# Optimization experiments

Measured on AMD Instinct MI355X. Metric: run time of the kernel, lower is better.

The kernel has to match this reference:

```python
import jax, jax.numpy as jnp
import numpy as np

B, N, DIM = 4, 2048, 512
H, DH = 8, 64  # n_heads, dim_head; inner = H*DH = 512
SCALE = DH ** -0.5


def setup_inputs() -> dict:
    key = jax.random.key(0)
    k1, k2, k3 = jax.random.split(key, 3)
    inner = H * DH
    X = jax.random.normal(k1, (B, N, DIM), dtype=jnp.float32)
    W_qkv = jax.random.normal(k2, (DIM, 3 * inner), dtype=jnp.float32) * (DIM ** -0.5)
    W_out = jax.random.normal(k3, (inner, DIM), dtype=jnp.float32) * (inner ** -0.5)
    b_out = jnp.zeros((DIM,), dtype=jnp.float32)
    return {"X": X, "W_qkv": W_qkv, "W_out": W_out, "b_out": b_out}


def reference(X, W_qkv, W_out, b_out):
    # X: (b, n, dim)
    qkv = X @ W_qkv                      # (b, n, 3*h*d)
    q, k, v = jnp.split(qkv, 3, axis=-1)
    def to_heads(t):
        b, n, _ = t.shape
        return t.reshape(b, n, H, DH).transpose(0, 2, 1, 3)  # (b, h, n, d)
    q, k, v = to_heads(q), to_heads(k), to_heads(v)
    # NOTE: original computes scores[n, m] = k_n . q_m and softmaxes over m (query axis)
    scores = jnp.einsum('bhnd,bhmd->bhnm', k, q) * SCALE     # (b, h, n_k, m_q)
    att = jax.nn.softmax(scores, axis=-1)
    # out token axis is the KEY index n: out[n, d] = sum_e att[n, e] * v[e, d]
    out = jnp.einsum('bhne,bhed->bhnd', att, v)              # (b, h, n, d)
    out = out.transpose(0, 2, 1, 3).reshape(X.shape[0], X.shape[1], H * DH)  # (b, n, h*d)
    return out @ W_out + b_out
```

## Files before the change

### kernel.cpp

```cpp
#include <hip/hip_runtime.h>
#include <hip/hip_bf16.h>

typedef __bf16 bf16_t;
typedef bf16_t bf16x8 __attribute__((ext_vector_type(8)));
typedef bf16_t bf16x4v __attribute__((ext_vector_type(4)));
typedef float f32x4 __attribute__((ext_vector_type(4)));

#define B_SZ 4
#define N_TOK 2048
#define DIM 512
#define H_N 8
#define DH 64
#define INNER 512
#define M_ROWS 8192
#define NQKV 1536
#define K_FOLD 0.18033688011112042f

#define GLD_LDS16(gp, lp)                                          \
  __builtin_amdgcn_global_load_lds(                                \
      (const __attribute__((address_space(1))) void*)(gp),         \
      (__attribute__((address_space(3))) void*)(lp), 16, 0, 0)

__device__ __forceinline__ float fexp2(float x) {
#if __has_builtin(__builtin_amdgcn_exp2f)
  return __builtin_amdgcn_exp2f(x);
#else
  float r;
  asm volatile("v_exp_f32 %0, %1\n\ts_nop 1" : "=v"(r) : "v"(x));
  return r;
#endif
}


__global__ void f32_to_bf16_kernel(const float* __restrict__ src,
                                   bf16_t* __restrict__ dst, int n4) {
  int i = blockIdx.x * blockDim.x + threadIdx.x;
  int stride = gridDim.x * blockDim.x;
  for (; i < n4; i += stride) {
    float4 f = reinterpret_cast<const float4*>(src)[i];
    bf16x4v o;
    o.x = (bf16_t)f.x; o.y = (bf16_t)f.y; o.z = (bf16_t)f.z; o.w = (bf16_t)f.w;
    reinterpret_cast<bf16x4v*>(dst)[i] = o;
  }
}

__global__ void transpose_f32_to_bf16_kernel(const float* __restrict__ src,
                                             bf16_t* __restrict__ dst, int R, int C) {
  int t = blockIdx.x * blockDim.x + threadIdx.x;
  if (t >= R * C) return;
  int r = t / C, c = t - r * C;
  dst[(size_t)c * R + r] = (bf16_t)src[t];
}

template <int MODE>
__global__ __launch_bounds__(256) void gemm_bf16_kernel(
    const bf16_t* __restrict__ A, const bf16_t* __restrict__ Bt,
    int M, int Nn, int K,
    bf16_t* __restrict__ qb, bf16_t* __restrict__ kb, bf16_t* __restrict__ vb,
    float* __restrict__ outF, const float* __restrict__ bias) {
  __shared__ bf16_t As[128 * 64];
  __shared__ bf16_t Bs[128 * 64];

  const int tid = threadIdx.x;
  const int lane = tid & 63;
  const int wave = tid >> 6;
  const int g = lane >> 4, c = lane & 15;
  const int wm = (wave >> 1) * 64, wn = (wave & 1) * 64;
  const int m0 = blockIdx.x * 128, n0 = blockIdx.y * 128;

  f32x4 acc[4][4] = {};

  for (int k0 = 0; k0 < K; k0 += 64) {
    __syncthreads();
    #pragma unroll
    for (int i = 0; i < 4; ++i) {
      int blk = i * 256 + tid;
      int row = blk >> 3;
      int cb = (blk & 7) ^ (row & 7);
      int base = (i * 256 + wave * 64) * 8;
      GLD_LDS16(A + (size_t)(m0 + row) * K + k0 + cb * 8, &As[base]);
      GLD_LDS16(Bt + (size_t)(n0 + row) * K + k0 + cb * 8, &Bs[base]);
    }
    __syncthreads();
    __builtin_amdgcn_s_setprio(1);
    #pragma unroll
    for (int ks = 0; ks < 2; ++ks) {
      bf16x8 af[4], bfr[4];
      #pragma unroll
      for (int i = 0; i < 4; ++i) {
        af[i] = *reinterpret_cast<const bf16x8*>(
            &As[(wm + i * 16 + c) * 64 + (((ks * 4 + g) ^ (c & 7)) * 8)]);
        bfr[i] = *reinterpret_cast<const bf16x8*>(
            &Bs[(wn + i * 16 + c) * 64 + (((ks * 4 + g) ^ (c & 7)) * 8)]);
      }
      #pragma unroll
      for (int mi = 0; mi < 4; ++mi)
        #pragma unroll
        for (int ni = 0; ni < 4; ++ni)
          acc[mi][ni] = __builtin_amdgcn_mfma_f32_16x16x32_bf16(
              af[mi], bfr[ni], acc[mi][ni], 0, 0, 0);
    }
    __builtin_amdgcn_s_setprio(0);
  }

  #pragma unroll
  for (int mi = 0; mi < 4; ++mi) {
    #pragma unroll
    for (int ni = 0; ni < 4; ++ni) {
      int colg = n0 + wn + ni * 16 + c;
      #pragma unroll
      for (int r = 0; r < 4; ++r) {
        int rowg = m0 + wm + mi * 16 + g * 4 + r;
        float val = acc[mi][ni][r];
        if (MODE == 0) {
          int s = colg >> 9, cc2 = colg & 511;
          int hh = cc2 >> 6, dd = cc2 & 63;
          int bb = rowg >> 11, nn = rowg & 2047;
          if (s == 1) val *= K_FOLD;
          bf16_t* dst = (s == 0) ? qb : (s == 1) ? kb : vb;
          dst[(((size_t)(bb * H_N + hh)) * N_TOK + nn) * DH + dd] = (bf16_t)val;
        } else {
          outF[(size_t)rowg * Nn + colg] = val + bias[colg];
        }
      }
    }
  }
}

__global__ __launch_bounds__(256) void vtrans_kernel(const bf16_t* __restrict__ V,
                                                     bf16_t* __restrict__ Vt) {
  const int nb = blockIdx.x, bh = blockIdx.y;
  const bf16_t* src = V + (size_t)bh * N_TOK * DH;
  bf16_t* dst = Vt + (size_t)bh * DH * N_TOK;
  __shared__ bf16_t t[64][64];
  const int tid = threadIdx.x;
  #pragma unroll
  for (int i = 0; i < 2; ++i) {
    int idx = tid + 256 * i;
    int r = idx >> 3, j = idx & 7;
    int cx = (j ^ (r & 7) ^ (r >> 3)) * 8;
    *reinterpret_cast<uint4*>(&t[r][cx]) =
        *reinterpret_cast<const uint4*>(&src[(size_t)(nb * 64 + r) * DH + j * 8]);
  }
  __syncthreads();
  #pragma unroll
  for (int i = 0; i < 2; ++i) {
    int idx = tid + 256 * i;
    int d = idx >> 3, jn = idx & 7;
    bf16_t tmp[8];
    #pragma unroll
    for (int q = 0; q < 8; ++q)
      tmp[q] = t[jn * 8 + q][(((d >> 3) ^ q ^ jn) * 8) | (d & 7)];
    *reinterpret_cast<uint4*>(&dst[(size_t)d * N_TOK + nb * 64 + jn * 8]) =
        *reinterpret_cast<const uint4*>(tmp);
  }
}

__global__ __launch_bounds__(512, 4) void attn_kernel(
    const bf16_t* __restrict__ Qproj, const bf16_t* __restrict__ Kproj,
    const bf16_t* __restrict__ Vt, bf16_t* __restrict__ att_out) {
  const int glin = blockIdx.x;
  const int xcd = glin & 7;
  const int j = glin >> 3;
  const int hb = xcd * 4 + (j >> 4);
  const int rb = j & 15;
  const int h = hb & 7, b = hb >> 3;

  const size_t hbo = (size_t)(b * H_N + h);
  const bf16_t* Aq = Kproj + hbo * N_TOK * DH;
  const bf16_t* Ak = Qproj + hbo * N_TOK * DH;
  const bf16_t* Av = Vt + hbo * (size_t)DH * N_TOK;

  const int tid = threadIdx.x, lane = tid & 63, wave = tid >> 6;
  const int g = lane >> 4, c = lane & 15;
  const int r0 = rb * 128, wr0 = wave * 16;

  __shared__ bf16_t sK[2][64 * 64];
  __shared__ bf16_t sV[2][64 * 64];
  __shared__ bf16_t sP[8][16 * 72];

  bf16x8 qreg[2];
  #pragma unroll
  for (int ks = 0; ks < 2; ++ks)
    qreg[ks] = *reinterpret_cast<const bf16x8*>(
        &Aq[(size_t)(r0 + wr0 + c) * DH + ks * 32 + g * 8]);

  f32x4 accO[4] = {};
  float Lp[4] = {0.f, 0.f, 0.f, 0.f};

  auto stage = [&](int buf, int j0) {
    int row = tid >> 3;
    int cb = (tid & 7) ^ (row & 7);
    GLD_LDS16(Ak + (size_t)(j0 + row) * DH + cb * 8, &sK[buf][wave * 512]);
    GLD_LDS16(Av + (size_t)row * N_TOK + j0 + cb * 8, &sV[buf][wave * 512]);
  };

  stage(0, 0);
  __syncthreads();
  int cur = 0;
  for (int t = 0; t < N_TOK / 64; ++t) {
    if (t + 1 < N_TOK / 64) stage(cur ^ 1, (t + 1) * 64);
    const bf16_t* bK = sK[cur];
    const bf16_t* bV = sV[cur];

    f32x4 accT[4] = {};
    __builtin_amdgcn_s_setprio(1);
    #pragma unroll
    for (int ks = 0; ks < 2; ++ks) {
      bf16x8 ak[4];
      #pragma unroll
      for (int mi = 0; mi < 4; ++mi)
        ak[mi] = *reinterpret_cast<const bf16x8*>(
            &bK[(mi * 16 + c) * 64 + (((ks * 4 + g) ^ (c & 7)) * 8)]);
      #pragma unroll
      for (int mi = 0; mi < 4; ++mi)
        accT[mi] = __builtin_amdgcn_mfma_f32_16x16x32_bf16(
            ak[mi], qreg[ks], accT[mi], 0, 0, 0);
    }
    __builtin_amdgcn_s_setprio(0);

    #pragma unroll
    for (int mi = 0; mi < 4; ++mi) {
      float p0 = fexp2(accT[mi][0]);
      float p1 = fexp2(accT[mi][1]);
      float p2 = fexp2(accT[mi][2]);
      float p3 = fexp2(accT[mi][3]);
      Lp[mi] += (p0 + p1) + (p2 + p3);
      bf16x4v pk;
      pk.x = (bf16_t)p0; pk.y = (bf16_t)p1; pk.z = (bf16_t)p2; pk.w = (bf16_t)p3;
      *reinterpret_cast<bf16x4v*>(&sP[wave][c * 72 + mi * 16 + g * 4]) = pk;
    }

    __builtin_amdgcn_s_setprio(1);
    #pragma unroll
    for (int ks = 0; ks < 2; ++ks) {
      bf16x8 pa = *reinterpret_cast<const bf16x8*>(
          &sP[wave][c * 72 + ks * 32 + g * 8]);
      #pragma unroll
      for (int di = 0; di < 4; ++di) {
        bf16x8 vb = *reinterpret_cast<const bf16x8*>(
            &bV[(di * 16 + c) * 64 + (((ks * 4 + g) ^ (c & 7)) * 8)]);
        accO[di] = __builtin_amdgcn_mfma_f32_16x16x32_bf16(pa, vb, accO[di], 0, 0, 0);
      }
    }
    __builtin_amdgcn_s_setprio(0);
    __syncthreads();
    cur ^= 1;
  }

  float l = (Lp[0] + Lp[1]) + (Lp[2] + Lp[3]);
  l += __shfl_xor(l, 16);
  l += __shfl_xor(l, 32);
  float invL = 1.0f / l;
  #pragma unroll
  for (int r = 0; r < 4; ++r) {
    float inv = __shfl(invL, g * 4 + r);
    int row = r0 + wr0 + g * 4 + r;
    #pragma unroll
    for (int di = 0; di < 4; ++di) {
      int col = h * DH + di * 16 + c;
      att_out[((size_t)(b * N_TOK) + row) * INNER + col] =
          (bf16_t)(accO[di][r] * inv);
    }
  }
}


extern "C" void kernel_launch(void* const* d_in, const int* in_sizes, int n_in,
                              void* d_out, int out_size, void* d_ws, size_t ws_size,
                              hipStream_t stream) {
  const float* X    = (const float*)d_in[0];
  const float* Wqkv = (const float*)d_in[1];
  const float* Wout = (const float*)d_in[2];
  const float* bout = (const float*)d_in[3];
  float* out = (float*)d_out;

  char* ws = (char*)d_ws;
  bf16_t* Xb    = (bf16_t*)(ws);
  bf16_t* WqkvT = (bf16_t*)(ws + 8388608);
  bf16_t* WoutT = (bf16_t*)(ws + 9961472);
  bf16_t* Qb    = (bf16_t*)(ws + 10485760);
  bf16_t* Kb    = (bf16_t*)(ws + 18874368);
  bf16_t* Vb    = (bf16_t*)(ws + 27262976);
  bf16_t* AttO  = (bf16_t*)(ws + 35651584);
  bf16_t* Vt    = Xb;

  f32_to_bf16_kernel<<<2048, 256, 0, stream>>>(X, Xb, (M_ROWS * DIM) / 4);
  transpose_f32_to_bf16_kernel<<<(DIM * NQKV + 255) / 256, 256, 0, stream>>>(
      Wqkv, WqkvT, DIM, NQKV);
  transpose_f32_to_bf16_kernel<<<(INNER * DIM + 255) / 256, 256, 0, stream>>>(
      Wout, WoutT, INNER, DIM);

  dim3 g1(M_ROWS / 128, NQKV / 128);
  gemm_bf16_kernel<0><<<g1, 256, 0, stream>>>(Xb, WqkvT, M_ROWS, NQKV, DIM,
                                              Qb, Kb, Vb, nullptr, nullptr);

  dim3 gv(N_TOK / 64, B_SZ * H_N);
  vtrans_kernel<<<gv, 256, 0, stream>>>(Vb, Vt);

  attn_kernel<<<dim3(512), 512, 0, stream>>>(Qb, Kb, Vt, AttO);

  dim3 g3(M_ROWS / 128, DIM / 128);
  gemm_bf16_kernel<1><<<g3, 256, 0, stream>>>(AttO, WoutT, M_ROWS, DIM, DIM,
                                              nullptr, nullptr, nullptr, out, bout);
}
```

Before: 97.85 us.

## Write V transposed from QKV GEMM epilogue and software-pipeline PV MFMA in attention

The QKV GEMM epilogue now writes the V section directly in transposed (d-major) layout with packed 4-element stores, which removes the separate vtrans kernel launch and its global round trip. The attention loop is restructured so that the P·V MFMAs for tile t-1 run alongside the QK^T MFMAs for tile t. This uses a double-buffered P tile per wave and a triple-buffered V tile in LDS, and leaves one barrier per iteration. The cost is more LDS per block, which may affect occupancy, and a strided 8-byte transposed store pattern in the GEMM epilogue.

```diff
diff --git a/kernel.cpp b/kernel.cpp
--- a/kernel.cpp
+++ b/kernel.cpp
@@ -56,7 +56,7 @@
 __global__ __launch_bounds__(256) void gemm_bf16_kernel(
     const bf16_t* __restrict__ A, const bf16_t* __restrict__ Bt,
     int M, int Nn, int K,
-    bf16_t* __restrict__ qb, bf16_t* __restrict__ kb, bf16_t* __restrict__ vb,
+    bf16_t* __restrict__ qb, bf16_t* __restrict__ kb, bf16_t* __restrict__ vtb,
     float* __restrict__ outF, const float* __restrict__ bias) {
   __shared__ bf16_t As[128 * 64];
   __shared__ bf16_t Bs[128 * 64];
@@ -108,51 +108,35 @@
     #pragma unroll
     for (int ni = 0; ni < 4; ++ni) {
       int colg = n0 + wn + ni * 16 + c;
-      #pragma unroll
-      for (int r = 0; r < 4; ++r) {
-        int rowg = m0 + wm + mi * 16 + g * 4 + r;
-        float val = acc[mi][ni][r];
-        if (MODE == 0) {
-          int s = colg >> 9, cc2 = colg & 511;
-          int hh = cc2 >> 6, dd = cc2 & 63;
-          int bb = rowg >> 11, nn = rowg & 2047;
-          if (s == 1) val *= K_FOLD;
-          bf16_t* dst = (s == 0) ? qb : (s == 1) ? kb : vb;
-          dst[(((size_t)(bb * H_N + hh)) * N_TOK + nn) * DH + dd] = (bf16_t)val;
+      if (MODE == 0) {
+        int s = colg >> 9;
+        int hh = (colg >> 6) & 7, dd = colg & 63;
+        int rowg0 = m0 + wm + mi * 16 + g * 4;
+        int bb = rowg0 >> 11, nn = rowg0 & 2047;
+        if (s == 2) {
+          bf16x4v pk;
+          pk.x = (bf16_t)acc[mi][ni][0];
+          pk.y = (bf16_t)acc[mi][ni][1];
+          pk.z = (bf16_t)acc[mi][ni][2];
+          pk.w = (bf16_t)acc[mi][ni][3];
+          *reinterpret_cast<bf16x4v*>(
+              &vtb[(((size_t)(bb * H_N + hh)) * DH + dd) * N_TOK + nn]) = pk;
         } else {
-          outF[(size_t)rowg * Nn + colg] = val + bias[colg];
+          float sc = (s == 1) ? K_FOLD : 1.0f;
+          bf16_t* dst = (s == 0) ? qb : kb;
+          #pragma unroll
+          for (int r = 0; r < 4; ++r)
+            dst[(((size_t)(bb * H_N + hh)) * N_TOK + nn + r) * DH + dd] =
+                (bf16_t)(acc[mi][ni][r] * sc);
+        }
+      } else {
+        #pragma unroll
+        for (int r = 0; r < 4; ++r) {
+          int rowg = m0 + wm + mi * 16 + g * 4 + r;
+          outF[(size_t)rowg * Nn + colg] = acc[mi][ni][r] + bias[colg];
         }
       }
     }
-  }
-}
-
-__global__ __launch_bounds__(256) void vtrans_kernel(const bf16_t* __restrict__ V,
-                                                     bf16_t* __restrict__ Vt) {
-  const int nb = blockIdx.x, bh = blockIdx.y;
-  const bf16_t* src = V + (size_t)bh * N_TOK * DH;
-  bf16_t* dst = Vt + (size_t)bh * DH * N_TOK;
-  __shared__ bf16_t t[64][64];
-  const int tid = threadIdx.x;
-  #pragma unroll
-  for (int i = 0; i < 2; ++i) {
-    int idx = tid + 256 * i;
-    int r = idx >> 3, j = idx & 7;
-    int cx = (j ^ (r & 7) ^ (r >> 3)) * 8;
-    *reinterpret_cast<uint4*>(&t[r][cx]) =
-        *reinterpret_cast<const uint4*>(&src[(size_t)(nb * 64 + r) * DH + j * 8]);
-  }
-  __syncthreads();
-  #pragma unroll
-  for (int i = 0; i < 2; ++i) {
-    int idx = tid + 256 * i;
-    int d = idx >> 3, jn = idx & 7;
-    bf16_t tmp[8];
-    #pragma unroll
-    for (int q = 0; q < 8; ++q)
-      tmp[q] = t[jn * 8 + q][(((d >> 3) ^ q ^ jn) * 8) | (d & 7)];
-    *reinterpret_cast<uint4*>(&dst[(size_t)d * N_TOK + nb * 64 + jn * 8]) =
-        *reinterpret_cast<const uint4*>(tmp);
   }
 }
 
@@ -176,8 +160,8 @@
   const int r0 = rb * 128, wr0 = wave * 16;
 
   __shared__ bf16_t sK[2][64 * 64];
-  __shared__ bf16_t sV[2][64 * 64];
-  __shared__ bf16_t sP[8][16 * 72];
+  __shared__ bf16_t sV[3][64 * 64];
+  __shared__ bf16_t sP[8][2][16 * 72];
 
   bf16x8 qreg[2];
   #pragma unroll
@@ -188,23 +172,32 @@
   f32x4 accO[4] = {};
   float Lp[4] = {0.f, 0.f, 0.f, 0.f};
 
-  auto stage = [&](int buf, int j0) {
-    int row = tid >> 3;
-    int cb = (tid & 7) ^ (row & 7);
-    GLD_LDS16(Ak + (size_t)(j0 + row) * DH + cb * 8, &sK[buf][wave * 512]);
-    GLD_LDS16(Av + (size_t)row * N_TOK + j0 + cb * 8, &sV[buf][wave * 512]);
+  const int srow = tid >> 3;
+  const int scb = (tid & 7) ^ (srow & 7);
+
+  auto stageK = [&](int buf, int j0) {
+    GLD_LDS16(Ak + (size_t)(j0 + srow) * DH + scb * 8, &sK[buf][wave * 512]);
   };
-
-  stage(0, 0);
+  auto stageV = [&](int buf, int j0) {
+    GLD_LDS16(Av + (size_t)srow * N_TOK + j0 + scb * 8, &sV[buf][wave * 512]);
+  };
+
+  stageK(0, 0);
+  stageV(0, 0);
   __syncthreads();
-  int cur = 0;
-  for (int t = 0; t < N_TOK / 64; ++t) {
-    if (t + 1 < N_TOK / 64) stage(cur ^ 1, (t + 1) * 64);
-    const bf16_t* bK = sK[cur];
-    const bf16_t* bV = sV[cur];
-
+
+  constexpr int NT = N_TOK / 64;
+  int vcur = 0, vold = 0;
+  for (int t = 0; t < NT; ++t) {
+    int vnext = (vcur == 2) ? 0 : vcur + 1;
+    if (t + 1 < NT) {
+      stageK((t + 1) & 1, (t + 1) * 64);
+      stageV(vnext, (t + 1) * 64);
+    }
+    const bf16_t* bK = sK[t & 1];
+
+    __builtin_amdgcn_s_setprio(1);
     f32x4 accT[4] = {};
-    __builtin_amdgcn_s_setprio(1);
     #pragma unroll
     for (int ks = 0; ks < 2; ++ks) {
       bf16x8 ak[4];
@@ -217,8 +210,24 @@
         accT[mi] = __builtin_amdgcn_mfma_f32_16x16x32_bf16(
             ak[mi], qreg[ks], accT[mi], 0, 0, 0);
     }
+
+    if (t > 0) {
+      const bf16_t* bV = sV[vold];
+      const bf16_t* pp = sP[wave][(t & 1) ^ 1];
+      #pragma unroll
+      for (int ks = 0; ks < 2; ++ks) {
+        bf16x8 pa = *reinterpret_cast<const bf16x8*>(&pp[c * 72 + ks * 32 + g * 8]);
+        #pragma unroll
+        for (int di = 0; di < 4; ++di) {
+          bf16x8 vv = *reinterpret_cast<const bf16x8*>(
+              &bV[(di * 16 + c) * 64 + (((ks * 4 + g) ^ (c & 7)) * 8)]);
+          accO[di] = __builtin_amdgcn_mfma_f32_16x16x32_bf16(pa, vv, accO[di], 0, 0, 0);
+        }
+      }
+    }
     __builtin_amdgcn_s_setprio(0);
 
+    bf16_t* pw = sP[wave][t & 1];
     #pragma unroll
     for (int mi = 0; mi < 4; ++mi) {
       float p0 = fexp2(accT[mi][0]);
@@ -228,24 +237,27 @@
       Lp[mi] += (p0 + p1) + (p2 + p3);
       bf16x4v pk;
       pk.x = (bf16_t)p0; pk.y = (bf16_t)p1; pk.z = (bf16_t)p2; pk.w = (bf16_t)p3;
-      *reinterpret_cast<bf16x4v*>(&sP[wave][c * 72 + mi * 16 + g * 4]) = pk;
-    }
-
-    __builtin_amdgcn_s_setprio(1);
+      *reinterpret_cast<bf16x4v*>(&pw[c * 72 + mi * 16 + g * 4]) = pk;
+    }
+
+    __syncthreads();
+    vold = vcur;
+    vcur = vnext;
+  }
+
+  {
+    const bf16_t* bV = sV[vold];
+    const bf16_t* pp = sP[wave][(NT - 1) & 1];
     #pragma unroll
     for (int ks = 0; ks < 2; ++ks) {
-      bf16x8 pa = *reinterpret_cast<const bf16x8*>(
-          &sP[wave][c * 72 + ks * 32 + g * 8]);
+      bf16x8 pa = *reinterpret_cast<const bf16x8*>(&pp[c * 72 + ks * 32 + g * 8]);
       #pragma unroll
       for (int di = 0; di < 4; ++di) {
-        bf16x8 vb = *reinterpret_cast<const bf16x8*>(
+        bf16x8 vv = *reinterpret_cast<const bf16x8*>(
             &bV[(di * 16 + c) * 64 + (((ks * 4 + g) ^ (c & 7)) * 8)]);
-        accO[di] = __builtin_amdgcn_mfma_f32_16x16x32_bf16(pa, vb, accO[di], 0, 0, 0);
+        accO[di] = __builtin_amdgcn_mfma_f32_16x16x32_bf16(pa, vv, accO[di], 0, 0, 0);
       }
     }
-    __builtin_amdgcn_s_setprio(0);
-    __syncthreads();
-    cur ^= 1;
   }
 
   float l = (Lp[0] + Lp[1]) + (Lp[2] + Lp[3]);
@@ -281,9 +293,8 @@
   bf16_t* WoutT = (bf16_t*)(ws + 9961472);
   bf16_t* Qb    = (bf16_t*)(ws + 10485760);
   bf16_t* Kb    = (bf16_t*)(ws + 18874368);
-  bf16_t* Vb    = (bf16_t*)(ws + 27262976);
+  bf16_t* Vtb   = (bf16_t*)(ws + 27262976);
   bf16_t* AttO  = (bf16_t*)(ws + 35651584);
-  bf16_t* Vt    = Xb;
 
   f32_to_bf16_kernel<<<2048, 256, 0, stream>>>(X, Xb, (M_ROWS * DIM) / 4);
   transpose_f32_to_bf16_kernel<<<(DIM * NQKV + 255) / 256, 256, 0, stream>>>(
@@ -293,12 +304,9 @@
 
   dim3 g1(M_ROWS / 128, NQKV / 128);
   gemm_bf16_kernel<0><<<g1, 256, 0, stream>>>(Xb, WqkvT, M_ROWS, NQKV, DIM,
-                                              Qb, Kb, Vb, nullptr, nullptr);
-
-  dim3 gv(N_TOK / 64, B_SZ * H_N);
-  vtrans_kernel<<<gv, 256, 0, stream>>>(Vb, Vt);
-
-  attn_kernel<<<dim3(512), 512, 0, stream>>>(Qb, Kb, Vt, AttO);
+                                              Qb, Kb, Vtb, nullptr, nullptr);
+
+  attn_kernel<<<dim3(512), 512, 0, stream>>>(Qb, Kb, Vtb, AttO);
 
   dim3 g3(M_ROWS / 128, DIM / 128);
   gemm_bf16_kernel<1><<<g3, 256, 0, stream>>>(AttO, WoutT, M_ROWS, DIM, DIM,
```

After: 94.08 us. -3.9%, faster.
